# Performance work log

Hardware: AMD Instinct MI355X
Metric: run time of the kernel (lower is better)

Reference implementation:

```python
import jax, jax.numpy as jnp
import numpy as np

L = 50000          # n_agents - 1 neighbors
OBS = 256          # input_shape[0]
ACT = 64           # output_shape
OTHER = 512        # input_shape[1]
HID = 64           # rnn_hidden_dim (forced by attn shape: 64 + cate_dim)
CATE = 32          # cate_dim


def setup_inputs() -> dict:
    key = jax.random.key(0)
    ks = jax.random.split(key, 16)
    s = 0.05
    return {
        "inputs": jax.random.normal(ks[0], (OBS,), jnp.float32),
        "act_idx": jax.random.normal(ks[1], (ACT,), jnp.float32),
        "other_inputs": jax.random.normal(ks[2], (L, OTHER), jnp.float32),
        # fc11: Linear(OBS+ACT, 64)
        "W11": jax.random.normal(ks[3], (HID, OBS + ACT), jnp.float32) * s,
        "b11": jax.random.normal(ks[4], (HID,), jnp.float32) * s,
        # fc12: Linear(OTHER, CATE)
        "W12": jax.random.normal(ks[5], (CATE, OTHER), jnp.float32) * s,
        "b12": jax.random.normal(ks[6], (CATE,), jnp.float32) * s,
        # attn: Linear(HID+CATE, 1)
        "Wa": jax.random.normal(ks[7], (1, HID + CATE), jnp.float32) * s,
        "ba": jax.random.normal(ks[8], (1,), jnp.float32) * s,
        # attn_out: Linear(CATE, CATE)
        "Wao": jax.random.normal(ks[9], (CATE, CATE), jnp.float32) * s,
        "bao": jax.random.normal(ks[10], (CATE,), jnp.float32) * s,
        # fc2: Linear(HID+CATE, HID)
        "W2": jax.random.normal(ks[11], (HID, HID + CATE), jnp.float32) * s,
        "b2": jax.random.normal(ks[12], (HID,), jnp.float32) * s,
        # fc3: Linear(HID, 1)
        "W3": jax.random.normal(ks[13], (1, HID), jnp.float32) * s,
        "b3": jax.random.normal(ks[14], (1,), jnp.float32) * s,
    }


def reference(inputs, act_idx, other_inputs, W11, b11, W12, b12, Wa, ba, Wao, bao, W2, b2, W3, b3):
    # cat obs with one-hot-style action index vector (dim 0 of 1D tensors)
    x_in = jnp.concatenate([inputs, act_idx])            # [OBS+ACT]
    input_x = W11 @ x_in + b11                           # [HID]

    # per-neighbor embedding (vectorized over the L neighbors)
    emb = other_inputs @ W12.T + b12                     # [L, CATE]

    # attention score attn(relu(cat(input_x, emb_i))); relu is elementwise,
    # so split the attn weight into the input_x part and the emb part.
    rx = jax.nn.relu(input_x)                            # [HID]
    re = jax.nn.relu(emb)                                # [L, CATE]
    w = rx @ Wa[0, :HID] + re @ Wa[0, HID:] + ba[0]      # [L]
    aw = jax.nn.softmax(w)                               # softmax over neighbors

    # attention-weighted mixture of neighbor embeddings
    mixed = aw @ emb                                     # [CATE]
    mixed = jax.nn.relu(mixed) @ Wao.T + bao             # attn_out

    # straight-through categorical (argmax one-hot, soft gradient)
    z_prob = jax.nn.softmax(mixed)                       # [CATE]
    samples = jax.nn.one_hot(jnp.argmax(z_prob), CATE, dtype=z_prob.dtype)
    one_hot_st = samples + (z_prob - jax.lax.stop_gradient(z_prob))

    x = jax.nn.relu(jnp.concatenate([input_x, one_hot_st]))  # [HID+CATE]
    h = jax.nn.relu(W2 @ x + b2)                             # [HID]
    r = W3 @ h + b3                                          # [1]
    return (r, samples)
```

## Files before the change

### kernel.cpp

```cpp
#include <hip/hip_runtime.h>

#define L_N    50000
#define K_DIM  512
#define GRID1  256
#define NGRP   3125
#define SB()   __builtin_amdgcn_sched_barrier(0)

typedef __attribute__((ext_vector_type(8))) short bf16x8;
typedef __attribute__((ext_vector_type(4))) float f32x4;

__device__ __forceinline__ void split8(float4 a, float4 b, bf16x8& hi, bf16x8& lo) {
    float v[8] = {a.x, a.y, a.z, a.w, b.x, b.y, b.z, b.w};
    #pragma unroll
    for (int j = 0; j < 8; ++j) {
        unsigned u  = __float_as_uint(v[j]);
        unsigned hb = u & 0xFFFF0000u;
        float    lf = v[j] - __uint_as_float(hb);
        hi[j] = (short)(hb >> 16);
        lo[j] = (short)(__float_as_uint(lf) >> 16);
    }
}

__global__ __launch_bounds__(1024) void k_part(
    const float* __restrict__ other,
    const float* __restrict__ W12,
    const float* __restrict__ b12,
    const float* __restrict__ Wa,
    float* __restrict__ ws)
{
    __shared__ short whi[16384];
    __shared__ short wlo[16384];
    __shared__ float sbuf[16][34];

    const int tid  = threadIdx.x;
    const int lane = tid & 63;
    const int wv   = tid >> 6;
    const int cl   = lane & 15;
    const int g    = lane >> 4;

    #pragma unroll
    for (int c2 = 0; c2 < 2; ++c2) {
        const int u  = tid + c2 * 1024;
        const int ch = u >> 6, r = u & 63;
        const float* wp = W12 + (size_t)ch * K_DIM + (r >> 2) * 32 + (r & 3) * 4;
        const float4 f0 = *(const float4*)wp;
        const float4 f1 = *(const float4*)(wp + 16);
        bf16x8 h8, l8; split8(f0, f1, h8, l8);
        const int p = (r * 32 + (ch ^ (r & 31))) * 8;
        *(bf16x8*)&whi[p] = h8;
        *(bf16x8*)&wlo[p] = l8;
    }
    __syncthreads();

    float rps = 0.f, rm0 = 0.f, rm1 = 0.f;
    const int wid = blockIdx.x * 16 + wv;

    if (wid < NGRP) {
        const float b0 = b12[cl],     b1 = b12[16 + cl];
        const float w0 = Wa[64 + cl], w1 = Wa[80 + cl];

        const float* xp = other + (size_t)(wid * 16 + cl) * K_DIM + (g << 2);

        float4 a0, a1, a2, a3, b0v, b1v, b2v, b3v, c0v, c1v, c2v, c3v, d0v, d1v, d2v, d3v;

        #define GLD(dst, OFF)                                                  \
            asm volatile("global_load_dwordx4 %0, %1, off offset:" OFF        \
                         : "=v"(dst) : "v"(xp) : "memory")
        #define GLDQ(x0,x1,x2,x3, O0,O1,O2,O3) do {                            \
            GLD(x0, O0); GLD(x1, O1); GLD(x2, O2); GLD(x3, O3);                \
        } while (0)
        #define VMW(N) do {                                                    \
            asm volatile("s_waitcnt vmcnt(" #N ")" ::: "memory");              \
            __builtin_amdgcn_sched_barrier(0);    \
        } while (0)

        f32x4 acc0 = {0.f,0.f,0.f,0.f}, acc1 = {0.f,0.f,0.f,0.f};

        #define CONSH(xlo, xhi, KC) do {                                       \
            bf16x8 ah, al; split8(xlo, xhi, ah, al);                           \
            const int r_  = (KC) * 4 + g;                                      \
            const int u0_ = (r_ * 32 + (cl ^ (r_ & 31))) * 8;                  \
            const bf16x8 bh0 = *(const bf16x8*)&whi[u0_];                      \
            const bf16x8 bl0 = *(const bf16x8*)&wlo[u0_];                      \
            const bf16x8 bh1 = *(const bf16x8*)&whi[u0_ ^ 128];                \
            const bf16x8 bl1 = *(const bf16x8*)&wlo[u0_ ^ 128];                \
            acc0 = __builtin_amdgcn_mfma_f32_16x16x32_bf16(ah, bh0, acc0, 0, 0, 0); \
            acc0 = __builtin_amdgcn_mfma_f32_16x16x32_bf16(al, bh0, acc0, 0, 0, 0); \
            acc0 = __builtin_amdgcn_mfma_f32_16x16x32_bf16(ah, bl0, acc0, 0, 0, 0); \
            acc1 = __builtin_amdgcn_mfma_f32_16x16x32_bf16(ah, bh1, acc1, 0, 0, 0); \
            acc1 = __builtin_amdgcn_mfma_f32_16x16x32_bf16(al, bh1, acc1, 0, 0, 0); \
            acc1 = __builtin_amdgcn_mfma_f32_16x16x32_bf16(ah, bl1, acc1, 0, 0, 0); \
        } while (0)
        #define CONSQ(x0,x1,x2,x3, QQ) do {                                    \
            CONSH(x0, x1, 2*(QQ));                                             \
            CONSH(x2, x3, 2*(QQ)+1);                                           \
        } while (0)

        GLDQ(a0,a1,a2,a3,   "0",   "64",  "128",  "192");
        GLDQ(b0v,b1v,b2v,b3v, "256",  "320",  "384",  "448");
        GLDQ(c0v,c1v,c2v,c3v, "512",  "576",  "640",  "704");
        GLDQ(d0v,d1v,d2v,d3v, "768",  "832",  "896",  "960");
        VMW(12); CONSQ(a0,a1,a2,a3, 0);  GLDQ(a0,a1,a2,a3, "1024","1088","1152","1216");
        VMW(12); CONSQ(b0v,b1v,b2v,b3v, 1); GLDQ(b0v,b1v,b2v,b3v, "1280","1344","1408","1472");
        VMW(12); CONSQ(c0v,c1v,c2v,c3v, 2); GLDQ(c0v,c1v,c2v,c3v, "1536","1600","1664","1728");
        VMW(12); CONSQ(d0v,d1v,d2v,d3v, 3); GLDQ(d0v,d1v,d2v,d3v, "1792","1856","1920","1984");
        VMW(12); CONSQ(a0,a1,a2,a3, 4);
        VMW(8);  CONSQ(b0v,b1v,b2v,b3v, 5);
        VMW(4);  CONSQ(c0v,c1v,c2v,c3v, 6);
        VMW(0);  CONSQ(d0v,d1v,d2v,d3v, 7);

        float e0[4], e1[4], s4[4];
        #pragma unroll
        for (int i = 0; i < 4; ++i) {
            e0[i] = acc0[i] + b0;
            e1[i] = acc1[i] + b1;
            s4[i] = fmaxf(e0[i], 0.f) * w0 + fmaxf(e1[i], 0.f) * w1;
        }
        #pragma unroll
        for (int d = 1; d < 16; d <<= 1) {
            #pragma unroll
            for (int i = 0; i < 4; ++i) s4[i] += __shfl_xor(s4[i], d);
        }
        #pragma unroll
        for (int i = 0; i < 4; ++i) {
            const float p = __expf(s4[i]);
            rps += p;
            rm0 = fmaf(p, e0[i], rm0);
            rm1 = fmaf(p, e1[i], rm1);
        }
    }

    rps += __shfl_xor(rps, 16); rps += __shfl_xor(rps, 32);
    rm0 += __shfl_xor(rm0, 16); rm0 += __shfl_xor(rm0, 32);
    rm1 += __shfl_xor(rm1, 16); rm1 += __shfl_xor(rm1, 32);
    if (lane == 0)  sbuf[wv][0] = rps;
    if (lane < 16) { sbuf[wv][1 + cl] = rm0; sbuf[wv][17 + cl] = rm1; }
    __syncthreads();
    if (wv == 0 && lane < 33) {
        float v = 0.f;
        #pragma unroll
        for (int s = 0; s < 16; ++s) v += sbuf[s][lane];
        ws[lane * GRID1 + blockIdx.x] = v;
    }
}

__global__ __launch_bounds__(256) void k_final(
    const float* __restrict__ ws,
    const float* __restrict__ inputs,
    const float* __restrict__ act_idx,
    const float* __restrict__ W11, const float* __restrict__ b11,
    const float* __restrict__ Wao, const float* __restrict__ bao,
    const float* __restrict__ W2,  const float* __restrict__ b2,
    const float* __restrict__ W3,  const float* __restrict__ b3,
    float* __restrict__ out)
{
    __shared__ float xsin[320];
    __shared__ float wsl[33];
    __shared__ float rm[32], z[32], xcat[96], h64[64];
    __shared__ int   amax;

    const int t = threadIdx.x, hh = t >> 2, q = t & 3;

    if (t < 132) {
        const int c = t >> 2, seg = t & 3;
        const float4* p = (const float4*)(ws + c * GRID1 + seg * 64);
        float v = 0.f;
        #pragma unroll
        for (int i = 0; i < 16; ++i) { const float4 f = p[i]; v += f.x + f.y + f.z + f.w; }
        v += __shfl_xor(v, 1);
        v += __shfl_xor(v, 2);
        if (seg == 0) wsl[c] = v;
    }
    xsin[t] = inputs[t];
    if (t < 64) xsin[256 + t] = act_idx[t];
    __syncthreads();

    if (t < 32) rm[t] = fmaxf(wsl[1 + t] / wsl[0], 0.f);

    float bp = 0.f;
    {
        const float4* wrow = (const float4*)(W11 + hh * 320 + q * 80);
        #pragma unroll
        for (int i = 0; i < 20; ++i) {
            const float4 f = wrow[i];
            const int k = q * 80 + i * 4;
            bp = fmaf(f.x, xsin[k], bp);
            bp = fmaf(f.y, xsin[k + 1], bp);
            bp = fmaf(f.z, xsin[k + 2], bp);
            bp = fmaf(f.w, xsin[k + 3], bp);
        }
    }
    bp += __shfl_xor(bp, 1);
    bp += __shfl_xor(bp, 2);
    __syncthreads();

    if (t < 32) {
        float zz = bao[t];
        for (int d = 0; d < 32; ++d) zz = fmaf(Wao[t * 32 + d], rm[d], zz);
        z[t] = zz;
    }
    __syncthreads();
    if (t == 0) {
        int bi = 0; float bv = z[0];
        for (int c = 1; c < 32; ++c) { if (z[c] > bv) { bv = z[c]; bi = c; } }
        amax = bi;
    }
    __syncthreads();
    if (q == 0) xcat[hh] = fmaxf(bp + b11[hh], 0.f);
    if (t < 32) xcat[64 + t] = (t == amax) ? 1.f : 0.f;
    __syncthreads();

    float dp = 0.f;
    for (int i = 0; i < 24; ++i) {
        const int k = q * 24 + i;
        dp = fmaf(W2[hh * 96 + k], xcat[k], dp);
    }
    dp += __shfl_xor(dp, 1);
    dp += __shfl_xor(dp, 2);
    if (q == 0) h64[hh] = fmaxf(dp + b2[hh], 0.f);
    __syncthreads();

    if (t == 0) {
        float r = b3[0];
        for (int i = 0; i < 64; ++i) r = fmaf(W3[i], h64[i], r);
        out[0] = r;
    }
    if (t < 32) out[1 + t] = (t == amax) ? 1.f : 0.f;
}

extern "C" void kernel_launch(void* const* d_in, const int* in_sizes, int n_in,
                              void* d_out, int out_size, void* d_ws, size_t ws_size,
                              hipStream_t stream) {
    const float* inputs  = (const float*)d_in[0];
    const float* act_idx = (const float*)d_in[1];
    const float* other   = (const float*)d_in[2];
    const float* W11     = (const float*)d_in[3];
    const float* b11     = (const float*)d_in[4];
    const float* W12     = (const float*)d_in[5];
    const float* b12     = (const float*)d_in[6];
    const float* Wa      = (const float*)d_in[7];
    const float* Wao     = (const float*)d_in[9];
    const float* bao     = (const float*)d_in[10];
    const float* W2      = (const float*)d_in[11];
    const float* b2      = (const float*)d_in[12];
    const float* W3      = (const float*)d_in[13];
    const float* b3      = (const float*)d_in[14];
    float* ws = (float*)d_ws;

    k_part<<<GRID1, 1024, 0, stream>>>(other, W12, b12, Wa, ws);
    k_final<<<1, 256, 0, stream>>>(ws, inputs, act_idx, W11, b11,
                                   Wao, bao, W2, b2, W3, b3, (float*)d_out);
}
```

Measured before the change: 32.33 us.

## Fuse final reduction into main kernel via last-block election and prefetch before weight staging

```diff
diff --git a/kernel.cpp b/kernel.cpp
--- a/kernel.cpp
+++ b/kernel.cpp
@@ -4,6 +4,7 @@
 #define K_DIM  512
 #define GRID1  256
 #define NGRP   3125
+#define NSLOT  16
 #define SB()   __builtin_amdgcn_sched_barrier(0)
 
 typedef __attribute__((ext_vector_type(8))) short bf16x8;
@@ -21,22 +22,51 @@
     }
 }
 
-__global__ __launch_bounds__(1024) void k_part(
+__global__ __launch_bounds__(1024) void k_fused(
     const float* __restrict__ other,
     const float* __restrict__ W12,
     const float* __restrict__ b12,
     const float* __restrict__ Wa,
-    float* __restrict__ ws)
+    const float* __restrict__ inputs,
+    const float* __restrict__ act_idx,
+    const float* __restrict__ W11, const float* __restrict__ b11,
+    const float* __restrict__ Wao, const float* __restrict__ bao,
+    const float* __restrict__ W2,  const float* __restrict__ b2,
+    const float* __restrict__ W3,  const float* __restrict__ b3,
+    float* __restrict__ ws,
+    float* __restrict__ out)
 {
     __shared__ short whi[16384];
     __shared__ short wlo[16384];
     __shared__ float sbuf[16][34];
+    __shared__ int   elect;
 
     const int tid  = threadIdx.x;
     const int lane = tid & 63;
     const int wv   = tid >> 6;
     const int cl   = lane & 15;
     const int g    = lane >> 4;
+    const int wid  = blockIdx.x * 16 + wv;
+    const bool act = (wid < NGRP);
+
+    const float* xp = other + (size_t)((act ? wid : 0) * 16 + cl) * K_DIM + (g << 2);
+
+    float4 a0, a1, a2, a3, b0v, b1v, b2v, b3v, c0v, c1v, c2v, c3v, d0v, d1v, d2v, d3v;
+
+    #define GLD(dst, OFF)                                                  \
+        asm volatile("global_load_dwordx4 %0, %1, off offset:" OFF        \
+                     : "=v"(dst) : "v"(xp) : "memory")
+    #define GLDQ(x0,x1,x2,x3, O0,O1,O2,O3) do {                            \
+        GLD(x0, O0); GLD(x1, O1); GLD(x2, O2); GLD(x3, O3);                \
+    } while (0)
+    #define VMW(N) do {                                                    \
+        asm volatile("s_waitcnt vmcnt(" #N ")" ::: "memory");              \
+        __builtin_amdgcn_sched_barrier(0);                    \
+    } while (0)
+
+    GLDQ(a0,a1,a2,a3,     "0",   "64",  "128",  "192");
+    GLDQ(b0v,b1v,b2v,b3v, "256", "320", "384",  "448");
+    SB();
 
     #pragma unroll
     for (int c2 = 0; c2 < 2; ++c2) {
@@ -53,26 +83,10 @@
     __syncthreads();
 
     float rps = 0.f, rm0 = 0.f, rm1 = 0.f;
-    const int wid = blockIdx.x * 16 + wv;
-
-    if (wid < NGRP) {
+
+    if (act) {
         const float b0 = b12[cl],     b1 = b12[16 + cl];
         const float w0 = Wa[64 + cl], w1 = Wa[80 + cl];
-
-        const float* xp = other + (size_t)(wid * 16 + cl) * K_DIM + (g << 2);
-
-        float4 a0, a1, a2, a3, b0v, b1v, b2v, b3v, c0v, c1v, c2v, c3v, d0v, d1v, d2v, d3v;
-
-        #define GLD(dst, OFF)                                                  \
-            asm volatile("global_load_dwordx4 %0, %1, off offset:" OFF        \
-                         : "=v"(dst) : "v"(xp) : "memory")
-        #define GLDQ(x0,x1,x2,x3, O0,O1,O2,O3) do {                            \
-            GLD(x0, O0); GLD(x1, O1); GLD(x2, O2); GLD(x3, O3);                \
-        } while (0)
-        #define VMW(N) do {                                                    \
-            asm volatile("s_waitcnt vmcnt(" #N ")" ::: "memory");              \
-            __builtin_amdgcn_sched_barrier(0);    \
-        } while (0)
 
         f32x4 acc0 = {0.f,0.f,0.f,0.f}, acc1 = {0.f,0.f,0.f,0.f};
 
@@ -96,12 +110,11 @@
             CONSH(x2, x3, 2*(QQ)+1);                                           \
         } while (0)
 
-        GLDQ(a0,a1,a2,a3,   "0",   "64",  "128",  "192");
-        GLDQ(b0v,b1v,b2v,b3v, "256",  "320",  "384",  "448");
         GLDQ(c0v,c1v,c2v,c3v, "512",  "576",  "640",  "704");
         GLDQ(d0v,d1v,d2v,d3v, "768",  "832",  "896",  "960");
-        VMW(12); CONSQ(a0,a1,a2,a3, 0);  GLDQ(a0,a1,a2,a3, "1024","1088","1152","1216");
-        VMW(12); CONSQ(b0v,b1v,b2v,b3v, 1); GLDQ(b0v,b1v,b2v,b3v, "1280","1344","1408","1472");
+        VMW(8);
+        CONSQ(a0,a1,a2,a3, 0);      GLDQ(a0,a1,a2,a3, "1024","1088","1152","1216");
+        CONSQ(b0v,b1v,b2v,b3v, 1);  GLDQ(b0v,b1v,b2v,b3v, "1280","1344","1408","1472");
         VMW(12); CONSQ(c0v,c1v,c2v,c3v, 2); GLDQ(c0v,c1v,c2v,c3v, "1536","1600","1664","1728");
         VMW(12); CONSQ(d0v,d1v,d2v,d3v, 3); GLDQ(d0v,d1v,d2v,d3v, "1792","1856","1920","1984");
         VMW(12); CONSQ(a0,a1,a2,a3, 4);
@@ -128,6 +141,8 @@
             rm0 = fmaf(p, e0[i], rm0);
             rm1 = fmaf(p, e1[i], rm1);
         }
+    } else {
+        VMW(0);
     }
 
     rps += __shfl_xor(rps, 16); rps += __shfl_xor(rps, 32);
@@ -140,45 +155,41 @@
         float v = 0.f;
         #pragma unroll
         for (int s = 0; s < 16; ++s) v += sbuf[s][lane];
-        ws[lane * GRID1 + blockIdx.x] = v;
-    }
-}
-
-__global__ __launch_bounds__(256) void k_final(
-    const float* __restrict__ ws,
-    const float* __restrict__ inputs,
-    const float* __restrict__ act_idx,
-    const float* __restrict__ W11, const float* __restrict__ b11,
-    const float* __restrict__ Wao, const float* __restrict__ bao,
-    const float* __restrict__ W2,  const float* __restrict__ b2,
-    const float* __restrict__ W3,  const float* __restrict__ b3,
-    float* __restrict__ out)
-{
+        atomicAdd(ws + lane * NSLOT + (blockIdx.x & (NSLOT - 1)), v);
+        __threadfence();
+    }
+    __syncthreads();
+    if (tid == 0) {
+        const int v = __hip_atomic_fetch_add((int*)(ws + 33 * NSLOT), 1,
+                                             __ATOMIC_ACQ_REL, __HIP_MEMORY_SCOPE_AGENT);
+        elect = (v == GRID1 - 1);
+    }
+    __syncthreads();
+    if (!elect) return;
+
     __shared__ float xsin[320];
     __shared__ float wsl[33];
     __shared__ float rm[32], z[32], xcat[96], h64[64];
     __shared__ int   amax;
 
-    const int t = threadIdx.x, hh = t >> 2, q = t & 3;
-
-    if (t < 132) {
-        const int c = t >> 2, seg = t & 3;
-        const float4* p = (const float4*)(ws + c * GRID1 + seg * 64);
-        float v = 0.f;
-        #pragma unroll
-        for (int i = 0; i < 16; ++i) { const float4 f = p[i]; v += f.x + f.y + f.z + f.w; }
+    const int t = tid, hh = t >> 2, q = t & 3;
+    if (t < 33 * NSLOT) {
+        const int c = t >> 4, s = t & 15;
+        float v = atomicAdd(ws + c * NSLOT + s, 0.f);
         v += __shfl_xor(v, 1);
         v += __shfl_xor(v, 2);
-        if (seg == 0) wsl[c] = v;
-    }
-    xsin[t] = inputs[t];
-    if (t < 64) xsin[256 + t] = act_idx[t];
+        v += __shfl_xor(v, 4);
+        v += __shfl_xor(v, 8);
+        if (s == 0) wsl[c] = v;
+    }
+    if (t < 256) xsin[t] = inputs[t];
+    if (t < 64)  xsin[256 + t] = act_idx[t];
     __syncthreads();
 
     if (t < 32) rm[t] = fmaxf(wsl[1 + t] / wsl[0], 0.f);
 
     float bp = 0.f;
-    {
+    if (t < 256) {
         const float4* wrow = (const float4*)(W11 + hh * 320 + q * 80);
         #pragma unroll
         for (int i = 0; i < 20; ++i) {
@@ -189,9 +200,9 @@
             bp = fmaf(f.z, xsin[k + 2], bp);
             bp = fmaf(f.w, xsin[k + 3], bp);
         }
-    }
-    bp += __shfl_xor(bp, 1);
-    bp += __shfl_xor(bp, 2);
+        bp += __shfl_xor(bp, 1);
+        bp += __shfl_xor(bp, 2);
+    }
     __syncthreads();
 
     if (t < 32) {
@@ -206,18 +217,20 @@
         amax = bi;
     }
     __syncthreads();
-    if (q == 0) xcat[hh] = fmaxf(bp + b11[hh], 0.f);
+    if (t < 256 && q == 0) xcat[hh] = fmaxf(bp + b11[hh], 0.f);
     if (t < 32) xcat[64 + t] = (t == amax) ? 1.f : 0.f;
     __syncthreads();
 
     float dp = 0.f;
-    for (int i = 0; i < 24; ++i) {
-        const int k = q * 24 + i;
-        dp = fmaf(W2[hh * 96 + k], xcat[k], dp);
-    }
-    dp += __shfl_xor(dp, 1);
-    dp += __shfl_xor(dp, 2);
-    if (q == 0) h64[hh] = fmaxf(dp + b2[hh], 0.f);
+    if (t < 256) {
+        for (int i = 0; i < 24; ++i) {
+            const int k = q * 24 + i;
+            dp = fmaf(W2[hh * 96 + k], xcat[k], dp);
+        }
+        dp += __shfl_xor(dp, 1);
+        dp += __shfl_xor(dp, 2);
+        if (q == 0) h64[hh] = fmaxf(dp + b2[hh], 0.f);
+    }
     __syncthreads();
 
     if (t == 0) {
@@ -247,7 +260,9 @@
     const float* b3      = (const float*)d_in[14];
     float* ws = (float*)d_ws;
 
-    k_part<<<GRID1, 1024, 0, stream>>>(other, W12, b12, Wa, ws);
-    k_final<<<1, 256, 0, stream>>>(ws, inputs, act_idx, W11, b11,
-                                   Wao, bao, W2, b2, W3, b3, (float*)d_out);
+    hipMemsetAsync(ws, 0, (33 * NSLOT + 1) * sizeof(float), stream);
+    k_fused<<<GRID1, 1024, 0, stream>>>(other, W12, b12, Wa,
+                                        inputs, act_idx, W11, b11,
+                                        Wao, bao, W2, b2, W3, b3,
+                                        ws, (float*)d_out);
 }
```

Result: slower. 45.31 us (+40.1%).
